# Kernel tuning notes

Hardware: AMD Instinct MI355X
Metric: run time of the kernel (lower is better)

Reference implementation:

```python
import jax, jax.numpy as jnp
import numpy as np

M = 150        # AR2 tail-fit window
LAM = 1e-3     # ridge regularizer in the 2x2 solve
CLIP_K = 4.0   # soft clip multiplier
H = 96         # forecast horizon (base_model.H)


def setup_inputs() -> dict:
    key = jax.random.key(0)
    k1, k2 = jax.random.split(key)
    x = jax.random.normal(k1, (32, 512, 2048), dtype=jnp.float32)
    W = jax.random.normal(k2, (2048, 96), dtype=jnp.float32) * 0.02
    return {"x": x, "W": W}


def _ar2_forecast(x):
    # x: (B, C, L); closed-form AR2 fit on last M samples, vectorized over (B, C)
    y = x[..., -M:]                     # (B, C, M)
    Y = y[..., 2:]                      # targets
    p1 = y[..., 1:-1]
    p2 = y[..., :-2]
    s = lambda a, b: jnp.sum(a * b, axis=-1)
    A11 = s(p1, p1) + LAM
    A22 = s(p2, p2) + LAM
    A12 = s(p1, p2)
    b1 = s(p1, Y)
    b2 = s(p2, Y)
    det = A11 * A22 - A12 * A12
    a1 = (b1 * A22 - b2 * A12) / det    # (B, C)
    a2 = (A11 * b2 - A12 * b1) / det

    def step(carry, _):
        y1, y2 = carry
        yn = a1 * y1 + a2 * y2
        return (yn, y1), yn

    _, out = jax.lax.scan(step, (x[..., -1], x[..., -2]), None, length=H)
    return jnp.moveaxis(out, 0, -1)     # (B, C, H)


def reference(x, W):
    # AR2 part is computed on detached history in the original (numpy round-trip)
    Yb = jax.lax.stop_gradient(_ar2_forecast(x))
    d_hat = jnp.einsum('bcl,lh->bch', x, W)          # base model: per-channel linear head
    y_hat = Yb + d_hat
    last = x[..., -1:]                               # (B, C, 1), broadcasts over H
    hstd = jnp.maximum(jnp.std(x, axis=-1, ddof=1, keepdims=True), 1e-6)  # torch unbiased std
    return jnp.clip(y_hat, last - CLIP_K * hstd, last + CLIP_K * hstd)
```

## Files before the change

kernel.cpp:

```cpp
#include <hip/hip_runtime.h>
#include <math.h>

constexpr int L     = 2048;
constexpr int NH    = 96;
constexpr int MLEN  = 150;
constexpr int NAR   = 148;
constexpr float LAM    = 0.001f;
constexpr float CLIP_K = 4.0f;

constexpr int TM     = 32;
constexpr int KM     = 64;
constexpr int MSTEPS = L / KM;

typedef __attribute__((ext_vector_type(8))) short short8;
typedef __attribute__((ext_vector_type(4))) float floatx4;

__device__ inline short f2bf(float f) {
    union { float f; unsigned u; } v; v.f = f;
    unsigned r = v.u + 0x7FFFu + ((v.u >> 16) & 1u);
    return (short)(r >> 16);
}

__global__ __launch_bounds__(256) void wt_kernel(
    const float* __restrict__ W, short* __restrict__ Wt)
{
    int idx = blockIdx.x * 256 + threadIdx.x;
    int n = idx >> 11;
    int k = idx & 2047;
    Wt[idx] = f2bf(W[k * NH + n]);
}

__global__ __launch_bounds__(256) void gemm_ar2_kernel(
    const float* __restrict__ x, const short* __restrict__ Wt,
    float* __restrict__ out)
{
    __shared__ float As[2][TM * KM];
    __shared__ short Bs[2][NH * KM];
    __shared__ float Ys[TM][NH + 1];
    __shared__ float los[TM], his[TM];

    const int t    = threadIdx.x;
    const int lane = t & 63;
    const int wv   = t >> 6;
    const int h    = wv >> 1;
    const int g    = wv & 1;
    const int m    = lane & 15;
    const int quad = lane >> 4;
    const int row0 = blockIdx.x * TM;
    const int r    = h * 16 + m;

    const int cA0 = wv * 128 + lane, cA1 = cA0 + 64;
    const int rA0 = cA0 >> 4, chA0 = cA0 & 15;
    const int rA1 = cA1 >> 4, chA1 = cA1 & 15;
    const float* pa0 = x + (size_t)(row0 + rA0) * L
                         + ((chA0 >> 3) * 32 + ((chA0 & 7) ^ (rA0 & 7)) * 4);
    const float* pa1 = x + (size_t)(row0 + rA1) * L
                         + ((chA1 >> 3) * 32 + ((chA1 & 7) ^ (rA1 & 7)) * 4);

    const int cB0 = wv * 192 + lane, cB1 = cB0 + 64, cB2 = cB0 + 128;
    const short* pb0 = Wt + (size_t)(cB0 >> 3) * L + (((cB0 & 7) ^ ((cB0 >> 3) & 7)) * 8);
    const short* pb1 = Wt + (size_t)(cB1 >> 3) * L + (((cB1 & 7) ^ ((cB1 >> 3) & 7)) * 8);
    const short* pb2 = Wt + (size_t)(cB2 >> 3) * L + (((cB2 & 7) ^ ((cB2 >> 3) & 7)) * 8);

    floatx4 acc[3];
    #pragma unroll
    for (int jj = 0; jj < 3; ++jj) acc[jj] = floatx4{0.f, 0.f, 0.f, 0.f};
    float sum = 0.f, sumsq = 0.f;

    const int pA0 = (2 * quad)     ^ (m & 7);
    const int pA1 = (2 * quad + 1) ^ (m & 7);

    auto stage = [&](int buf, int k0) {
        __builtin_amdgcn_global_load_lds(
            (const __attribute__((address_space(1))) unsigned int*)(pa0 + k0),
            (__attribute__((address_space(3))) unsigned int*)&As[buf][wv * 512], 16, 0, 0);
        __builtin_amdgcn_global_load_lds(
            (const __attribute__((address_space(1))) unsigned int*)(pa1 + k0),
            (__attribute__((address_space(3))) unsigned int*)&As[buf][wv * 512 + 256], 16, 0, 0);
        __builtin_amdgcn_global_load_lds(
            (const __attribute__((address_space(1))) unsigned int*)(pb0 + k0),
            (__attribute__((address_space(3))) unsigned int*)&Bs[buf][wv * 1536], 16, 0, 0);
        __builtin_amdgcn_global_load_lds(
            (const __attribute__((address_space(1))) unsigned int*)(pb1 + k0),
            (__attribute__((address_space(3))) unsigned int*)&Bs[buf][wv * 1536 + 512], 16, 0, 0);
        __builtin_amdgcn_global_load_lds(
            (const __attribute__((address_space(1))) unsigned int*)(pb2 + k0),
            (__attribute__((address_space(3))) unsigned int*)&Bs[buf][wv * 1536 + 1024], 16, 0, 0);
    };

    stage(0, 0);

    for (int s = 0; s < MSTEPS; ++s) {
        const int cur = s & 1;
        __syncthreads();
        if (s + 1 < MSTEPS) stage(cur ^ 1, (s + 1) * KM);

        #pragma unroll
        for (int ss = 0; ss < 2; ++ss) {
            float4 f0 = *(const float4*)&As[cur][r * KM + ss * 32 + pA0 * 4];
            float4 f1 = *(const float4*)&As[cur][r * KM + ss * 32 + pA1 * 4];

            if (g == 0) {
                sum  += ((f0.x + f0.y) + (f0.z + f0.w))
                      + ((f1.x + f1.y) + (f1.z + f1.w));
                sumsq = fmaf(f0.x, f0.x, sumsq); sumsq = fmaf(f0.y, f0.y, sumsq);
                sumsq = fmaf(f0.z, f0.z, sumsq); sumsq = fmaf(f0.w, f0.w, sumsq);
                sumsq = fmaf(f1.x, f1.x, sumsq); sumsq = fmaf(f1.y, f1.y, sumsq);
                sumsq = fmaf(f1.z, f1.z, sumsq); sumsq = fmaf(f1.w, f1.w, sumsq);
            }

            short8 af;
            af[0] = f2bf(f0.x); af[1] = f2bf(f0.y); af[2] = f2bf(f0.z); af[3] = f2bf(f0.w);
            af[4] = f2bf(f1.x); af[5] = f2bf(f1.y); af[6] = f2bf(f1.z); af[7] = f2bf(f1.w);

            const int bch = ((ss * 4 + quad) ^ (m & 7)) * 8;
            #pragma unroll
            for (int jj = 0; jj < 3; ++jj) {
                short8 bf = *(const short8*)&Bs[cur][(g * 48 + jj * 16 + m) * KM + bch];
                acc[jj] = __builtin_amdgcn_mfma_f32_16x16x32_bf16(af, bf, acc[jj], 0, 0, 0);
            }
        }
    }

    if (g == 0) {
        sum   += __shfl_xor(sum,   16); sum   += __shfl_xor(sum,   32);
        sumsq += __shfl_xor(sumsq, 16); sumsq += __shfl_xor(sumsq, 32);

        const float* ytail = x + (size_t)(row0 + r) * L + (L - MLEN);
        float A11 = 0.f, A22 = 0.f, A12 = 0.f, b1 = 0.f, b2 = 0.f;
        for (int i = quad; i < NAR; i += 4) {
            float p2v = ytail[i];
            float p1v = ytail[i + 1];
            float Yv  = ytail[i + 2];
            A11 = fmaf(p1v, p1v, A11);
            A22 = fmaf(p2v, p2v, A22);
            A12 = fmaf(p1v, p2v, A12);
            b1  = fmaf(p1v, Yv,  b1);
            b2  = fmaf(p2v, Yv,  b2);
        }
        A11 += __shfl_xor(A11, 16); A11 += __shfl_xor(A11, 32);
        A22 += __shfl_xor(A22, 16); A22 += __shfl_xor(A22, 32);
        A12 += __shfl_xor(A12, 16); A12 += __shfl_xor(A12, 32);
        b1  += __shfl_xor(b1,  16); b1  += __shfl_xor(b1,  32);
        b2  += __shfl_xor(b2,  16); b2  += __shfl_xor(b2,  32);

        if (quad == 0) {
            A11 += LAM; A22 += LAM;
            float det = A11 * A22 - A12 * A12;
            float a1c = (b1 * A22 - b2 * A12) / det;
            float a2c = (A11 * b2 - A12 * b1) / det;

            float last = ytail[MLEN - 1];
            float y1 = last;
            float y2 = ytail[MLEN - 2];
            for (int n = 0; n < NH; ++n) {
                float yn = a1c * y1 + a2c * y2;
                Ys[r][n] = yn;
                y2 = y1; y1 = yn;
            }
            float var  = (sumsq - sum * sum * (1.0f / L)) * (1.0f / (L - 1));
            float hstd = fmaxf(sqrtf(fmaxf(var, 0.f)), 1e-6f);
            los[r] = last - CLIP_K * hstd;
            his[r] = last + CLIP_K * hstd;
        }
    }
    __syncthreads();

    #pragma unroll
    for (int reg = 0; reg < 4; ++reg) {
        int rl = h * 16 + quad * 4 + reg;
        float lo = los[rl], hi = his[rl];
        #pragma unroll
        for (int jj = 0; jj < 3; ++jj) {
            int c = (3 * g + jj) * 16 + m;
            float v = acc[jj][reg] + Ys[rl][c];
            v = fminf(fmaxf(v, lo), hi);
            out[(size_t)(row0 + rl) * NH + c] = v;
        }
    }
}

extern "C" void kernel_launch(void* const* d_in, const int* in_sizes, int n_in,
                              void* d_out, int out_size, void* d_ws, size_t ws_size,
                              hipStream_t stream) {
    const float* x = (const float*)d_in[0];
    const float* W = (const float*)d_in[1];
    float* out = (float*)d_out;
    short* Wt  = (short*)d_ws;

    wt_kernel<<<dim3((NH * L) / 256), dim3(256), 0, stream>>>(W, Wt);

    const int rows = 32 * 512;
    gemm_ar2_kernel<<<dim3(rows / TM), dim3(256), 0, stream>>>(x, Wt, out);
}
```

Before: 205.9 us.

## Double row tile to 64 with 512-thread blocks and reuse A buffer for AR2 forecasts

Doubles the rows per block from 32 to 64 and the threads per block from 256 to 512 (8 waves). Each W tile staged in LDS is now shared by twice as many rows, which halves the per-row B-operand load traffic. The Ys forecast buffer is dropped and the forecasts are written into the A staging buffer after an extra barrier, which keeps LDS use down. In exchange the grid has half as many blocks (256 instead of 512), the AR2 epilogue still runs serially on a few lanes, and some waves sit idle during the B staging loads.

```diff
diff --git a/kernel.cpp b/kernel.cpp
--- a/kernel.cpp
+++ b/kernel.cpp
@@ -8,7 +8,7 @@
 constexpr float LAM    = 0.001f;
 constexpr float CLIP_K = 4.0f;
 
-constexpr int TM     = 32;
+constexpr int TM     = 64;
 constexpr int KM     = 64;
 constexpr int MSTEPS = L / KM;
 
@@ -30,13 +30,12 @@
     Wt[idx] = f2bf(W[k * NH + n]);
 }
 
-__global__ __launch_bounds__(256) void gemm_ar2_kernel(
+__global__ __launch_bounds__(512) void gemm_ar2_kernel(
     const float* __restrict__ x, const short* __restrict__ Wt,
     float* __restrict__ out)
 {
     __shared__ float As[2][TM * KM];
     __shared__ short Bs[2][NH * KM];
-    __shared__ float Ys[TM][NH + 1];
     __shared__ float los[TM], his[TM];
 
     const int t    = threadIdx.x;
@@ -48,8 +47,9 @@
     const int quad = lane >> 4;
     const int row0 = blockIdx.x * TM;
     const int r    = h * 16 + m;
+    const int m7   = m & 7;
 
-    const int cA0 = wv * 128 + lane, cA1 = cA0 + 64;
+    const int cA0 = (wv * 2) * 64 + lane, cA1 = cA0 + 64;
     const int rA0 = cA0 >> 4, chA0 = cA0 & 15;
     const int rA1 = cA1 >> 4, chA1 = cA1 & 15;
     const float* pa0 = x + (size_t)(row0 + rA0) * L
@@ -57,38 +57,35 @@
     const float* pa1 = x + (size_t)(row0 + rA1) * L
                          + ((chA1 >> 3) * 32 + ((chA1 & 7) ^ (rA1 & 7)) * 4);
 
-    const int cB0 = wv * 192 + lane, cB1 = cB0 + 64, cB2 = cB0 + 128;
+    const int cB0 = wv * 64 + lane;
+    const int cB1 = (8 + wv) * 64 + lane;
     const short* pb0 = Wt + (size_t)(cB0 >> 3) * L + (((cB0 & 7) ^ ((cB0 >> 3) & 7)) * 8);
     const short* pb1 = Wt + (size_t)(cB1 >> 3) * L + (((cB1 & 7) ^ ((cB1 >> 3) & 7)) * 8);
-    const short* pb2 = Wt + (size_t)(cB2 >> 3) * L + (((cB2 & 7) ^ ((cB2 >> 3) & 7)) * 8);
 
     floatx4 acc[3];
     #pragma unroll
     for (int jj = 0; jj < 3; ++jj) acc[jj] = floatx4{0.f, 0.f, 0.f, 0.f};
     float sum = 0.f, sumsq = 0.f;
 
-    const int pA0 = (2 * quad)     ^ (m & 7);
-    const int pA1 = (2 * quad + 1) ^ (m & 7);
-
     auto stage = [&](int buf, int k0) {
         __builtin_amdgcn_global_load_lds(
             (const __attribute__((address_space(1))) unsigned int*)(pa0 + k0),
-            (__attribute__((address_space(3))) unsigned int*)&As[buf][wv * 512], 16, 0, 0);
+            (__attribute__((address_space(3))) unsigned int*)&As[buf][(wv * 2) * 256], 16, 0, 0);
         __builtin_amdgcn_global_load_lds(
             (const __attribute__((address_space(1))) unsigned int*)(pa1 + k0),
-            (__attribute__((address_space(3))) unsigned int*)&As[buf][wv * 512 + 256], 16, 0, 0);
+            (__attribute__((address_space(3))) unsigned int*)&As[buf][(wv * 2 + 1) * 256], 16, 0, 0);
         __builtin_amdgcn_global_load_lds(
             (const __attribute__((address_space(1))) unsigned int*)(pb0 + k0),
-            (__attribute__((address_space(3))) unsigned int*)&Bs[buf][wv * 1536], 16, 0, 0);
-        __builtin_amdgcn_global_load_lds(
-            (const __attribute__((address_space(1))) unsigned int*)(pb1 + k0),
-            (__attribute__((address_space(3))) unsigned int*)&Bs[buf][wv * 1536 + 512], 16, 0, 0);
-        __builtin_amdgcn_global_load_lds(
-            (const __attribute__((address_space(1))) unsigned int*)(pb2 + k0),
-            (__attribute__((address_space(3))) unsigned int*)&Bs[buf][wv * 1536 + 1024], 16, 0, 0);
+            (__attribute__((address_space(3))) unsigned int*)&Bs[buf][wv * 512], 16, 0, 0);
+        if (wv < 4)
+            __builtin_amdgcn_global_load_lds(
+                (const __attribute__((address_space(1))) unsigned int*)(pb1 + k0),
+                (__attribute__((address_space(3))) unsigned int*)&Bs[buf][(8 + wv) * 512], 16, 0, 0);
     };
 
     stage(0, 0);
+
+    const int pA0 = (2 * quad) ^ m7, pA1 = (2 * quad + 1) ^ m7;
 
     for (int s = 0; s < MSTEPS; ++s) {
         const int cur = s & 1;
@@ -113,7 +110,7 @@
             af[0] = f2bf(f0.x); af[1] = f2bf(f0.y); af[2] = f2bf(f0.z); af[3] = f2bf(f0.w);
             af[4] = f2bf(f1.x); af[5] = f2bf(f1.y); af[6] = f2bf(f1.z); af[7] = f2bf(f1.w);
 
-            const int bch = ((ss * 4 + quad) ^ (m & 7)) * 8;
+            const int bch = ((ss * 4 + quad) ^ m7) * 8;
             #pragma unroll
             for (int jj = 0; jj < 3; ++jj) {
                 short8 bf = *(const short8*)&Bs[cur][(g * 48 + jj * 16 + m) * KM + bch];
@@ -122,6 +119,7 @@
         }
     }
 
+    float a1c = 0.f, a2c = 0.f, last = 0.f, y2i = 0.f, lo = 0.f, hi = 0.f;
     if (g == 0) {
         sum   += __shfl_xor(sum,   16); sum   += __shfl_xor(sum,   32);
         sumsq += __shfl_xor(sumsq, 16); sumsq += __shfl_xor(sumsq, 32);
@@ -147,34 +145,40 @@
         if (quad == 0) {
             A11 += LAM; A22 += LAM;
             float det = A11 * A22 - A12 * A12;
-            float a1c = (b1 * A22 - b2 * A12) / det;
-            float a2c = (A11 * b2 - A12 * b1) / det;
-
-            float last = ytail[MLEN - 1];
-            float y1 = last;
-            float y2 = ytail[MLEN - 2];
-            for (int n = 0; n < NH; ++n) {
-                float yn = a1c * y1 + a2c * y2;
-                Ys[r][n] = yn;
-                y2 = y1; y1 = yn;
-            }
+            a1c = (b1 * A22 - b2 * A12) / det;
+            a2c = (A11 * b2 - A12 * b1) / det;
+            last = ytail[MLEN - 1];
+            y2i  = ytail[MLEN - 2];
             float var  = (sumsq - sum * sum * (1.0f / L)) * (1.0f / (L - 1));
             float hstd = fmaxf(sqrtf(fmaxf(var, 0.f)), 1e-6f);
-            los[r] = last - CLIP_K * hstd;
-            his[r] = last + CLIP_K * hstd;
+            lo = last - CLIP_K * hstd;
+            hi = last + CLIP_K * hstd;
         }
+    }
+    __syncthreads();
+
+    float* YsF = (float*)As;
+    if (g == 0 && quad == 0) {
+        float y1 = last, y2 = y2i;
+        for (int n = 0; n < NH; ++n) {
+            float yn = a1c * y1 + a2c * y2;
+            YsF[r * (NH + 1) + n] = yn;
+            y2 = y1; y1 = yn;
+        }
+        los[r] = lo;
+        his[r] = hi;
     }
     __syncthreads();
 
     #pragma unroll
     for (int reg = 0; reg < 4; ++reg) {
         int rl = h * 16 + quad * 4 + reg;
-        float lo = los[rl], hi = his[rl];
+        float rlo = los[rl], rhi = his[rl];
         #pragma unroll
         for (int jj = 0; jj < 3; ++jj) {
             int c = (3 * g + jj) * 16 + m;
-            float v = acc[jj][reg] + Ys[rl][c];
-            v = fminf(fmaxf(v, lo), hi);
+            float v = acc[jj][reg] + YsF[rl * (NH + 1) + c];
+            v = fminf(fmaxf(v, rlo), rhi);
             out[(size_t)(row0 + rl) * NH + c] = v;
         }
     }
@@ -191,5 +195,5 @@
     wt_kernel<<<dim3((NH * L) / 256), dim3(256), 0, stream>>>(W, Wt);
 
     const int rows = 32 * 512;
-    gemm_ar2_kernel<<<dim3(rows / TM), dim3(256), 0, stream>>>(x, Wt, out);
+    gemm_ar2_kernel<<<dim3(rows / TM), dim3(512), 0, stream>>>(x, Wt, out);
 }
```

New measurement: 210.3 us. +2.1%, slower.
